# Optimization experiments

Measured on AMD Instinct MI355X. Metric: run time of the kernel, lower is better.

## Reference

```python
import jax, jax.numpy as jnp
import numpy as np
from functools import partial

B, INPUT_DIM, CHUNK, D, NLAYERS, FF, NCLS = 16, 20480, 10, 256, 4, 1024, 10
L = INPUT_DIM // CHUNK  # 2048
FILT_EMB, FILT_HID = 16, 64
EPS = 1e-5


def sinusoidal_pe(length, dim):
    pos = jnp.arange(length, dtype=jnp.float32)[:, None]
    div = jnp.exp(jnp.arange(0, dim, 2, dtype=jnp.float32) * (-np.log(10000.0) / dim))
    ang = pos * div  # (length, dim//2)
    pe = jnp.zeros((length, dim), dtype=jnp.float32)
    pe = pe.at[:, 0::2].set(jnp.sin(ang)).at[:, 1::2].set(jnp.cos(ang))
    return pe


def layernorm(x, g, b):
    mu = jnp.mean(x, axis=-1, keepdims=True)
    var = jnp.mean(jnp.square(x - mu), axis=-1, keepdims=True)
    return (x - mu) * jax.lax.rsqrt(var + EPS) * g + b


def setup_inputs() -> dict:
    key = jax.random.key(0)
    ks = iter(jax.random.split(key, 32))
    s = 0.02
    r = lambda shape: jax.random.normal(next(ks), shape, dtype=jnp.float32) * s
    inp = {
        'x': jax.random.normal(next(ks), (B, INPUT_DIM), dtype=jnp.float32),
        'inp_w': r((CHUNK, D)), 'inp_b': jnp.zeros((D,)),
        'in_proj_w': r((NLAYERS, D, 3 * D)), 'in_proj_b': jnp.zeros((NLAYERS, 3 * D)),
        'short_w': r((NLAYERS, D, 3)), 'short_b': jnp.zeros((NLAYERS, D)),
        'filt_w1': r((NLAYERS, FILT_EMB, FILT_HID)), 'filt_b1': jnp.zeros((NLAYERS, FILT_HID)),
        'filt_w2': r((NLAYERS, FILT_HID, D)), 'filt_b2': jnp.zeros((NLAYERS, D)),
        'out_w': r((NLAYERS, D, D)), 'out_b': jnp.zeros((NLAYERS, D)),
        'ln1_g': jnp.ones((NLAYERS, D)), 'ln1_b': jnp.zeros((NLAYERS, D)),
        'ln2_g': jnp.ones((NLAYERS, D)), 'ln2_b': jnp.zeros((NLAYERS, D)),
        'ffn_w1': r((NLAYERS, D, FF)), 'ffn_b1': jnp.zeros((NLAYERS, FF)),
        'ffn_w2': r((NLAYERS, FF, D)), 'ffn_b2': jnp.zeros((NLAYERS, D)),
        'norm_g': jnp.ones((D,)), 'norm_b': jnp.zeros((D,)),
        'cls_w': r((D, NCLS)), 'cls_b': jnp.zeros((NCLS,)),
    }
    return inp


def _hyena_op(u, in_w, in_b, sw, sb, fw1, fb1, fw2, fb2, ow, ob, pe16):
    # u: (B, L, D)
    proj = u @ in_w + in_b                       # (B, L, 3D)
    x0, x1, x2 = jnp.split(proj, 3, axis=-1)
    # depthwise short conv, kernel 3, same padding
    x0t = jnp.transpose(x0, (0, 2, 1))           # (B, D, L)
    x0c = jax.lax.conv_general_dilated(
        x0t, sw[:, None, :], window_strides=(1,), padding=[(1, 1)],
        feature_group_count=D, dimension_numbers=('NCH', 'OIH', 'NCH'))
    x0c = jnp.transpose(x0c + sb[None, :, None], (0, 2, 1))  # (B, L, D)
    # implicit long filter from positional MLP
    h = jax.nn.gelu(pe16 @ fw1 + fb1, approximate=False) @ fw2 + fb2  # (L, D)
    # FFT causal-style long conv (n = 2L)
    xf = jnp.fft.rfft(x0c, n=2 * L, axis=1)
    hf = jnp.fft.rfft(h, n=2 * L, axis=0)
    y = jnp.fft.irfft(xf * hf[None], n=2 * L, axis=1)[:, :L, :]
    y = y * x1 * x2                              # elementwise gating
    return y @ ow + ob


def reference(x, inp_w, inp_b, in_proj_w, in_proj_b, short_w, short_b,
              filt_w1, filt_b1, filt_w2, filt_b2, out_w, out_b,
              ln1_g, ln1_b, ln2_g, ln2_b, ffn_w1, ffn_b1, ffn_w2, ffn_b2,
              norm_g, norm_b, cls_w, cls_b):
    xs = x.reshape(B, L, CHUNK) @ inp_w + inp_b  # (B, L, D)
    xs = xs + sinusoidal_pe(L, D)[None]
    pe16 = sinusoidal_pe(L, FILT_EMB)
    for i in range(NLAYERS):
        h = _hyena_op(layernorm(xs, ln1_g[i], ln1_b[i]),
                      in_proj_w[i], in_proj_b[i], short_w[i], short_b[i],
                      filt_w1[i], filt_b1[i], filt_w2[i], filt_b2[i],
                      out_w[i], out_b[i], pe16)
        xs = xs + h
        z = layernorm(xs, ln2_g[i], ln2_b[i])
        z = jax.nn.gelu(z @ ffn_w1[i] + ffn_b1[i], approximate=False) @ ffn_w2[i] + ffn_b2[i]
        xs = xs + z
    pooled = layernorm(jnp.mean(xs, axis=1), norm_g, norm_b)
    return pooled @ cls_w + cls_b
```

## Files before the change

kernel.cpp:

```cpp
#include <hip/hip_runtime.h>
#include <math.h>

#define BB 16
#define LL 2048
#define CHUNK 10
#define DD 256
#define NLAYERS 4
#define FFD 1024
#define NCLS 10
#define HSTRC 2056

typedef short bf16x8 __attribute__((ext_vector_type(8)));
typedef short s16x4 __attribute__((ext_vector_type(4)));
typedef float f32x4 __attribute__((ext_vector_type(4)));

__device__ __forceinline__ unsigned short f2bf(float f) {
    unsigned int u = __builtin_bit_cast(unsigned int, f);
    u = (u + 0x7FFF + ((u >> 16) & 1)) >> 16;
    return (unsigned short)u;
}
__device__ __forceinline__ float bf2f(unsigned short s) {
    unsigned int u = ((unsigned int)s) << 16;
    return __builtin_bit_cast(float, u);
}
__device__ __forceinline__ float bfLO(unsigned v) { return __builtin_bit_cast(float, v << 16); }
__device__ __forceinline__ float bfHI(unsigned v) { return __builtin_bit_cast(float, v & 0xFFFF0000u); }

#define PADC(a) ((a) + ((a) >> 4))

__device__ __forceinline__ float2 cmulf(float2 a, float2 b) {
    return make_float2(fmaf(-a.y, b.y, a.x * b.x), fmaf(a.y, b.x, a.x * b.y));
}

#define GLL16(gsrc, ldst) \
    __builtin_amdgcn_global_load_lds((const __attribute__((address_space(1))) void*)(gsrc), \
                                     (__attribute__((address_space(3))) void*)(ldst), 16, 0, 0)

__global__ __launch_bounds__(256)
void embed_k(const float* __restrict__ x, const float* __restrict__ iw,
             const float* __restrict__ ib, float* __restrict__ xs)
{
    const int tid = threadIdx.x;
    const size_t row0 = (size_t)blockIdx.x * 8;
    const int i2 = (tid >> 1) * 2;
    const float div = expf(-0.03597789207803197f * (float)i2);
    float wcol[CHUNK];
#pragma unroll
    for (int c = 0; c < CHUNK; ++c) wcol[c] = iw[c * DD + tid];
    const float bv = ib[tid];
    for (int rr = 0; rr < 8; ++rr) {
        size_t row = row0 + rr;
        int l = (int)(row & (LL - 1));
        const float* xr = x + row * CHUNK;
        float acc = bv;
#pragma unroll
        for (int c = 0; c < CHUNK; ++c) acc += xr[c] * wcol[c];
        float sv, cv;
        sincosf((float)l * div, &sv, &cv);
        acc += (tid & 1) ? cv : sv;
        xs[row * DD + tid] = acc;
    }
}

__global__ __launch_bounds__(256)
void filt_k(const float* __restrict__ fw1, const float* __restrict__ fb1,
            const float* __restrict__ fw2, const float* __restrict__ fb2,
            float* __restrict__ hT)
{
    __shared__ float pe[16];
    __shared__ float hid[64];
    const int tid = threadIdx.x, l = blockIdx.x;
    if (tid < 16) {
        int i2 = (tid >> 1) * 2;
        float div = expf(-0.5756462732485114f * (float)i2);
        float sv, cv;
        sincosf((float)l * div, &sv, &cv);
        pe[tid] = (tid & 1) ? cv : sv;
    }
    __syncthreads();
    if (tid < 64) {
        float a = fb1[tid];
#pragma unroll
        for (int e = 0; e < 16; ++e) a += pe[e] * fw1[e * 64 + tid];
        hid[tid] = 0.5f * a * (1.0f + erff(a * 0.70710678118f));
    }
    __syncthreads();
    float a = fb2[tid];
#pragma unroll
    for (int h = 0; h < 64; ++h) a += hid[h] * fw2[h * DD + tid];
    hT[(size_t)tid * LL + l] = a;
}

__device__ __forceinline__ void dft4c(float2 a, float2 b, float2 c, float2 d,
                                      float2& F0, float2& F1, float2& F2, float2& F3)
{
    float t0r = a.x + c.x, t0i = a.y + c.y;
    float t1r = a.x - c.x, t1i = a.y - c.y;
    float t2r = b.x + d.x, t2i = b.y + d.y;
    float t3r = b.x - d.x, t3i = b.y - d.y;
    F0 = make_float2(t0r + t2r, t0i + t2i);
    F2 = make_float2(t0r - t2r, t0i - t2i);
    F1 = make_float2(t1r + t3i, t1i - t3r);
    F3 = make_float2(t1r - t3i, t1i + t3r);
}

template <int SH>
__device__ __forceinline__ void stage8ip(float2* __restrict__ A, int tid)
{
    constexpr int ST = 1 << SH;
    const int p = tid >> SH;
    const int q = tid & (ST - 1);
    float2 x0 = A[PADC(tid)];
    float2 x1 = A[PADC(tid + 256)];
    float2 x2 = A[PADC(tid + 512)];
    float2 x3 = A[PADC(tid + 768)];
    float2 x4 = A[PADC(tid + 1024)];
    float2 x5 = A[PADC(tid + 1280)];
    float2 x6 = A[PADC(tid + 1536)];
    float2 x7 = A[PADC(tid + 1792)];
    float2 E0, E1, E2, E3, O0, O1, O2, O3;
    dft4c(x0, x2, x4, x6, E0, E1, E2, E3);
    dft4c(x1, x3, x5, x7, O0, O1, O2, O3);
    const float C8 = 0.70710678118654752f;
    float2 y0 = make_float2(E0.x + O0.x, E0.y + O0.y);
    float2 y4 = make_float2(E0.x - O0.x, E0.y - O0.y);
    float a1 = C8 * (O1.x + O1.y), b1 = C8 * (O1.y - O1.x);
    float2 y1 = make_float2(E1.x + a1, E1.y + b1);
    float2 y5 = make_float2(E1.x - a1, E1.y - b1);
    float2 y2 = make_float2(E2.x + O2.y, E2.y - O2.x);
    float2 y6 = make_float2(E2.x - O2.y, E2.y + O2.x);
    float a3 = -C8 * (O3.x - O3.y), b3 = -C8 * (O3.x + O3.y);
    float2 y3 = make_float2(E3.x + a3, E3.y + b3);
    float2 y7 = make_float2(E3.x - a3, E3.y - b3);
    const int k0 = p << SH;
    float s1, c1;
    __sincosf(-3.0679615757712823e-3f * (float)k0, &s1, &c1);
    float2 w1 = make_float2(c1, s1);
    float2 w2 = cmulf(w1, w1);
    float2 w3 = cmulf(w2, w1);
    float2 w4 = cmulf(w2, w2);
    float2 w5 = cmulf(w3, w2);
    float2 w6 = cmulf(w3, w3);
    float2 w7 = cmulf(w4, w3);
    float2 o1 = cmulf(w1, y1);
    float2 o2 = cmulf(w2, y2);
    float2 o3 = cmulf(w3, y3);
    float2 o4 = cmulf(w4, y4);
    float2 o5 = cmulf(w5, y5);
    float2 o6 = cmulf(w6, y6);
    float2 o7 = cmulf(w7, y7);
    __syncthreads();
    const int ob = q + ((ST * p) << 3);
    A[PADC(ob)] = y0;
    A[PADC(ob + ST)] = o1;
    A[PADC(ob + 2 * ST)] = o2;
    A[PADC(ob + 3 * ST)] = o3;
    A[PADC(ob + 4 * ST)] = o4;
    A[PADC(ob + 5 * ST)] = o5;
    A[PADC(ob + 6 * ST)] = o6;
    A[PADC(ob + 7 * ST)] = o7;
    __syncthreads();
}

__device__ __forceinline__ void stage4fip(float2* __restrict__ A, int tid)
{
    float2 v[2][4];
#pragma unroll
    for (int jj = 0; jj < 2; ++jj) {
        int u = tid + (jj << 8);
        v[jj][0] = A[PADC(u)];
        v[jj][1] = A[PADC(u + 512)];
        v[jj][2] = A[PADC(u + 1024)];
        v[jj][3] = A[PADC(u + 1536)];
    }
    __syncthreads();
#pragma unroll
    for (int jj = 0; jj < 2; ++jj) {
        int u = tid + (jj << 8);
        float2 F0, F1, F2, F3;
        dft4c(v[jj][0], v[jj][1], v[jj][2], v[jj][3], F0, F1, F2, F3);
        A[PADC(u)] = F0;
        A[PADC(u + 512)] = F1;
        A[PADC(u + 1024)] = F2;
        A[PADC(u + 1536)] = F3;
    }
    __syncthreads();
}

__device__ __forceinline__ void fft2048ip(float2* __restrict__ A, int tid)
{
    stage8ip<0>(A, tid);
    stage8ip<3>(A, tid);
    stage8ip<6>(A, tid);
    stage4fip(A, tid);
}

__global__ __launch_bounds__(256)
void ffth_k(const float* __restrict__ hT, float2* __restrict__ Hf)
{
    __shared__ float2 A2[2176];
    const int tid = threadIdx.x, d = blockIdx.x;
    const float2* rowf = reinterpret_cast<const float2*>(hT + (size_t)d * LL);
#pragma unroll
    for (int j = 0; j < 4; ++j) {
        int u = tid + (j << 8);
        A2[PADC(u)] = rowf[u];
        A2[PADC(u + 1024)] = make_float2(0.0f, 0.0f);
    }
    __syncthreads();
    fft2048ip(A2, tid);
    float2* hf = Hf + (size_t)d * HSTRC;
#pragma unroll
    for (int j = 0; j < 4; ++j) {
        int k = 1 + tid + (j << 8);
        int m = 2048 - k;
        float2 zk = A2[PADC(k)], zm = A2[PADC(m)];
        float Er = 0.5f * (zk.x + zm.x), Ei = 0.5f * (zk.y - zm.y);
        float Or = 0.5f * (zk.y + zm.y), Oi = -0.5f * (zk.x - zm.x);
        float ts, tc;
        __sincosf(-1.5339807878856412e-3f * (float)k, &ts, &tc);
        float TOr = tc * Or - ts * Oi, TOi = tc * Oi + ts * Or;
        hf[k] = make_float2(Er + TOr, Ei + TOi);
        hf[m] = make_float2(Er - TOr, -(Ei - TOi));
    }
    if (tid == 0) {
        float2 z0 = A2[PADC(0)];
        hf[0] = make_float2(z0.x + z0.y, z0.x - z0.y);
    }
}

__global__ __launch_bounds__(256, 4)
void fftconv_k(const unsigned short* __restrict__ x0T, unsigned short* __restrict__ yT,
               const float2* __restrict__ Hf, const float* __restrict__ sw,
               const float* __restrict__ sb)
{
    __shared__ float2 A2[2176];
    const int tid = threadIdx.x;
    const int w = blockIdx.x;
    const int c = w & 7, s = w >> 3;
    const int d = c * 32 + (s & 31);
    const int b = s >> 5;
    const int blk = b * 256 + d;
    const float w0 = sw[d * 3], w1 = sw[d * 3 + 1], w2 = sw[d * 3 + 2];
    const float bv = sb[d];

    float* rawF = reinterpret_cast<float*>(A2);
    {
        const uint4* rowv = reinterpret_cast<const uint4*>(x0T + (size_t)blk * LL);
        uint4 ld = rowv[tid];
        int p = tid << 3;
        int lB = p & ~63;
        int p6 = p & 63;
        int fg = p6 >> 4;
        int m0 = (p6 >> 2) & 3;
        float4* d0 = reinterpret_cast<float4*>(rawF + lB + m0 * 16 + fg * 4);
        float4* d1 = reinterpret_cast<float4*>(rawF + lB + (m0 + 1) * 16 + fg * 4);
        *d0 = make_float4(bfLO(ld.x), bfHI(ld.x), bfLO(ld.y), bfHI(ld.y));
        *d1 = make_float4(bfLO(ld.z), bfHI(ld.z), bfLO(ld.w), bfHI(ld.w));
    }
    __syncthreads();
    float2 zv[4];
#pragma unroll
    for (int j = 0; j < 4; ++j) {
        int u = tid + (j << 8);
        float xm1 = (u == 0) ? 0.0f : rawF[2 * u - 1];
        float xc0 = rawF[2 * u];
        float xp1 = rawF[2 * u + 1];
        float xp2 = (u == 1023) ? 0.0f : rawF[2 * u + 2];
        zv[j].x = bv + w0 * xm1 + w1 * xc0 + w2 * xp1;
        zv[j].y = bv + w0 * xc0 + w1 * xp1 + w2 * xp2;
    }
    __syncthreads();
#pragma unroll
    for (int j = 0; j < 4; ++j) {
        int u = tid + (j << 8);
        A2[PADC(u)] = zv[j];
        A2[PADC(u + 1024)] = make_float2(0.0f, 0.0f);
    }
    __syncthreads();
    fft2048ip(A2, tid);
    const float2* hf = Hf + (size_t)d * HSTRC;
#pragma unroll
    for (int j = 0; j < 4; ++j) {
        int k = 1 + tid + (j << 8);
        int m = 2048 - k;
        float2 zk = A2[PADC(k)], zm = A2[PADC(m)];
        float Er = 0.5f * (zk.x + zm.x), Ei = 0.5f * (zk.y - zm.y);
        float Or = 0.5f * (zk.y + zm.y), Oi = -0.5f * (zk.x - zm.x);
        float ts, tc;
        __sincosf(-1.5339807878856412e-3f * (float)k, &ts, &tc);
        float TOr = tc * Or - ts * Oi, TOi = tc * Oi + ts * Or;
        float Xpr = Er + TOr, Xpi = Ei + TOi;
        float Xmr = Er - TOr, Xmi = Ei - TOi;
        float2 hk = hf[k], hm = hf[m];
        float Ykr = Xpr * hk.x - Xpi * hk.y, Yki = Xpr * hk.y + Xpi * hk.x;
        float Cr = Xmr * hm.x + Xmi * hm.y, Ci = Xmi * hm.x - Xmr * hm.y;
        float Pr = 0.5f * (Ykr + Cr), Pi = 0.5f * (Yki + Ci);
        float Gr = 0.5f * (Ykr - Cr), Gi = 0.5f * (Yki - Ci);
        float Qr = tc * Gr + ts * Gi, Qi = tc * Gi - ts * Gr;
        A2[PADC(k)] = make_float2(Pr - Qi, -(Pi + Qr));
        A2[PADC(m)] = make_float2(Pr + Qi, Pi - Qr);
    }
    if (tid == 0) {
        float2 z0 = A2[PADC(0)];
        float2 h0 = hf[0];
        float X0 = z0.x + z0.y, X2 = z0.x - z0.y;
        float Y0 = X0 * h0.x, Y2 = X2 * h0.y;
        float P = 0.5f * (Y0 + Y2), Q = 0.5f * (Y0 - Y2);
        A2[PADC(0)] = make_float2(P, -Q);
    }
    __syncthreads();
    fft2048ip(A2, tid);
    const float sc = 1.0f / 2048.0f;
    unsigned* yrow = reinterpret_cast<unsigned*>(yT + (size_t)blk * LL);
#pragma unroll
    for (int j = 0; j < 4; ++j) {
        int u = tid + (j << 8);
        float2 v = A2[PADC(u)];
        float e = v.x * sc, o = -v.y * sc;
        yrow[u] = (unsigned)f2bf(e) | ((unsigned)f2bf(o) << 16);
    }
}

__global__ __launch_bounds__(256)
void gate_k(const unsigned short* __restrict__ yTb, const unsigned short* __restrict__ px,
            unsigned short* __restrict__ yg)
{
    __shared__ float t[64][65];
    const int tid = threadIdx.x;
    const int blk = blockIdx.x;
    const int b = blk >> 7;
    const int dt = (blk >> 5) & 3;
    const int lt = blk & 31;
    const int d0 = dt << 6, l0 = lt << 6;
    const int r0 = tid >> 6, c = tid & 63;
    for (int rr = 0; rr < 16; ++rr) {
        int dl = rr * 4 + r0;
        t[dl][c] = bf2f(yTb[(((size_t)(b << 8) + d0 + dl) << 11) + l0 + c]);
    }
    __syncthreads();
    const int lid = tid & 63, lr = tid >> 6;
    for (int k = 0; k < 16; ++k) {
        int ll = k * 4 + lr;
        int l = l0 + ll;
        size_t pb = ((size_t)(b * LL + l)) * 512;
        float v = t[lid][ll];
        float x1 = bf2f(px[pb + d0 + lid]);
        float x2 = bf2f(px[pb + 256 + d0 + lid]);
        yg[((size_t)(b * LL + l)) * DD + d0 + lid] = f2bf(v * x1 * x2);
    }
}

__global__ __launch_bounds__(256)
void lncast_k(const float* __restrict__ xs, const float* __restrict__ g,
              const float* __restrict__ b, unsigned short* __restrict__ o)
{
    const int tid = threadIdx.x, lane = tid & 63, wave = tid >> 6;
    const size_t row = (size_t)blockIdx.x * 4 + wave;
    float4 v = reinterpret_cast<const float4*>(xs + row * DD)[lane];
    float s = v.x + v.y + v.z + v.w;
#pragma unroll
    for (int off = 32; off > 0; off >>= 1) s += __shfl_xor(s, off, 64);
    float mean = s * (1.0f / 256.0f);
    float e0 = v.x - mean, e1 = v.y - mean, e2 = v.z - mean, e3 = v.w - mean;
    float q = e0 * e0 + e1 * e1 + e2 * e2 + e3 * e3;
#pragma unroll
    for (int off = 32; off > 0; off >>= 1) q += __shfl_xor(q, off, 64);
    float rstd = rsqrtf(q * (1.0f / 256.0f) + 1e-5f);
    float4 gg = reinterpret_cast<const float4*>(g)[lane];
    float4 bb = reinterpret_cast<const float4*>(b)[lane];
    s16x4 r;
    r[0] = (short)f2bf(e0 * rstd * gg.x + bb.x);
    r[1] = (short)f2bf(e1 * rstd * gg.y + bb.y);
    r[2] = (short)f2bf(e2 * rstd * gg.z + bb.z);
    r[3] = (short)f2bf(e3 * rstd * gg.w + bb.w);
    *reinterpret_cast<s16x4*>(o + row * DD + lane * 4) = r;
}

__global__ __launch_bounds__(256)
void wcastT_k(const float* __restrict__ W, unsigned short* __restrict__ WT, int K, int N)
{
    __shared__ float t[32][33];
    const int tx = threadIdx.x & 31, ty = threadIdx.x >> 5;
    const int n0 = blockIdx.x * 32, k0 = blockIdx.y * 32;
#pragma unroll
    for (int j = 0; j < 4; ++j)
        t[ty + 8 * j][tx] = W[(size_t)(k0 + ty + 8 * j) * N + n0 + tx];
    __syncthreads();
#pragma unroll
    for (int j = 0; j < 4; ++j)
        WT[(size_t)(n0 + ty + 8 * j) * K + k0 + tx] = f2bf(t[tx][ty + 8 * j]);
}

template <int K, int N, int MODE>
__global__ __launch_bounds__(256)
void gemm_k(const unsigned short* __restrict__ A, const unsigned short* __restrict__ WT,
            const float* __restrict__ bias, void* __restrict__ outp, void* __restrict__ outp2)
{
    constexpr int C = N / 128;
    __shared__ unsigned short ldsA[8192];
    __shared__ unsigned short ldsB[8192];
    const int tid = threadIdx.x;
    const int lane = tid & 63, wid = tid >> 6;
    const int nwg = gridDim.x;
    const int w = blockIdx.x;
    const int logical = (w & 7) * (nwg >> 3) + (w >> 3);
    const int row0 = (logical / C) * 128;
    const int col0 = (logical % C) * 128;
    const int wm = (wid >> 1) * 64, wn = (wid & 1) * 64;
    const int fr = lane & 15, fg = lane >> 4;

    f32x4 acc[4][4];
#pragma unroll
    for (int n = 0; n < 4; ++n) {
        float bv = bias[col0 + wn + n * 16 + fr];
#pragma unroll
        for (int m = 0; m < 4; ++m) {
            acc[m][n][0] = bv; acc[m][n][1] = bv; acc[m][n][2] = bv; acc[m][n][3] = bv;
        }
    }

    const int srow = wid * 8 + (lane >> 3);
    const int sc = lane & 7;

    for (int kt = 0; kt < K / 64; ++kt) {
        const int k0 = kt * 64;
#pragma unroll
        for (int it = 0; it < 4; ++it) {
            int row = it * 32 + srow;
            int cs = sc ^ (row & 7);
            const char* ga = (const char*)(A + (size_t)(row0 + row) * K + k0) + cs * 16;
            const char* gb = (const char*)(WT + (size_t)(col0 + row) * K + k0) + cs * 16;
            GLL16(ga, (char*)ldsA + it * 4096 + wid * 1024);
            GLL16(gb, (char*)ldsB + it * 4096 + wid * 1024);
        }
        __syncthreads();
#pragma unroll
        for (int ks = 0; ks < 2; ++ks) {
            bf16x8 af[4], bf[4];
#pragma unroll
            for (int m = 0; m < 4; ++m) {
                int ar = wm + m * 16 + fr;
                int slot = (ks * 4 + fg) ^ (ar & 7);
                af[m] = *reinterpret_cast<const bf16x8*>(ldsA + ar * 64 + slot * 8);
            }
#pragma unroll
            for (int n = 0; n < 4; ++n) {
                int br = wn + n * 16 + fr;
                int slot = (ks * 4 + fg) ^ (br & 7);
                bf[n] = *reinterpret_cast<const bf16x8*>(ldsB + br * 64 + slot * 8);
            }
#pragma unroll
            for (int m = 0; m < 4; ++m)
#pragma unroll
                for (int n = 0; n < 4; ++n)
                    acc[m][n] = __builtin_amdgcn_mfma_f32_16x16x32_bf16(af[m], bf[n], acc[m][n], 0, 0, 0);
        }
        __syncthreads();
    }

    if constexpr (MODE == 3) {
        if (col0 < 256) {
            const int b = row0 >> 11;
            const int lb0 = (row0 & (LL - 1)) + wm;
#pragma unroll
            for (int n = 0; n < 4; ++n) {
                int dcol = col0 + wn + n * 16 + fr;
                unsigned short* dst = (unsigned short*)outp +
                    (((size_t)(b << 8) + dcol) << 11) + lb0 + fg * 16;
                unsigned pk[8];
#pragma unroll
                for (int q = 0; q < 8; ++q) {
                    int m = q >> 1, r0 = (q & 1) * 2;
                    pk[q] = (unsigned)f2bf(acc[m][n][r0]) | ((unsigned)f2bf(acc[m][n][r0 + 1]) << 16);
                }
                *reinterpret_cast<uint4*>(dst)     = make_uint4(pk[0], pk[1], pk[2], pk[3]);
                *reinterpret_cast<uint4*>(dst + 8) = make_uint4(pk[4], pk[5], pk[6], pk[7]);
            }
        } else {
            unsigned short* px = (unsigned short*)outp2;
#pragma unroll
            for (int m = 0; m < 4; ++m) {
                int gr = row0 + wm + m * 16 + fg * 4;
#pragma unroll
                for (int n = 0; n < 4; ++n) {
                    int gc = col0 - 256 + wn + n * 16 + fr;
#pragma unroll
                    for (int r = 0; r < 4; ++r)
                        px[(size_t)(gr + r) * 512 + gc] = f2bf(acc[m][n][r]);
                }
            }
        }
        return;
    }

#pragma unroll
    for (int m = 0; m < 4; ++m) {
        int gr = row0 + wm + m * 16 + fg * 4;
#pragma unroll
        for (int n = 0; n < 4; ++n) {
            int gc = col0 + wn + n * 16 + fr;
#pragma unroll
            for (int r = 0; r < 4; ++r) {
                float v = acc[m][n][r];
                if constexpr (MODE == 1) v = 0.5f * v * (1.0f + erff(v * 0.70710678118f));
                if constexpr (MODE <= 1) {
                    ((unsigned short*)outp)[(size_t)(gr + r) * N + gc] = f2bf(v);
                } else {
                    float* o = (float*)outp + (size_t)(gr + r) * N + gc;
                    *o += v;
                }
            }
        }
    }
}

template <int K>
__global__ __launch_bounds__(256)
void gemm_ln_k(const unsigned short* __restrict__ A, const unsigned short* __restrict__ WT,
               const float* __restrict__ bias, const float* __restrict__ lng,
               const float* __restrict__ lnb, float* __restrict__ xs,
               unsigned short* __restrict__ xln)
{
    __shared__ unsigned short ldsA[64 * 64];
    __shared__ unsigned short ldsB[256 * 64];
    const int tid = threadIdx.x;
    const int lane = tid & 63, wid = tid >> 6;
    const int nwg = gridDim.x;
    const int w = blockIdx.x;
    const int logical = (w & 7) * (nwg >> 3) + (w >> 3);
    const size_t row0 = (size_t)logical * 64;
    const int fr = lane & 15, fg = lane >> 4;

    f32x4 acc[16];
#pragma unroll
    for (int n = 0; n < 16; ++n) {
        float bv = bias[n * 16 + fr];
        acc[n][0] = bv; acc[n][1] = bv; acc[n][2] = bv; acc[n][3] = bv;
    }

    for (int kt = 0; kt < K / 64; ++kt) {
        const int k0 = kt * 64;
#pragma unroll
        for (int p = 0; p < 2; ++p) {
            int cch = p * 256 + tid;
            int row = cch >> 3;
            int cs = (cch & 7) ^ (row & 7);
            const char* ga = (const char*)(A + (row0 + row) * K + k0) + cs * 16;
            GLL16(ga, (char*)ldsA + p * 4096 + wid * 1024);
        }
#pragma unroll
        for (int p = 0; p < 8; ++p) {
            int cch = p * 256 + tid;
            int row = cch >> 3;
            int cs = (cch & 7) ^ (row & 7);
            const char* gb = (const char*)(WT + (size_t)row * K + k0) + cs * 16;
            GLL16(gb, (char*)ldsB + p * 4096 + wid * 1024);
        }
        __syncthreads();
#pragma unroll
        for (int ks = 0; ks < 2; ++ks) {
            int ar = wid * 16 + fr;
            int slotA = (ks * 4 + fg) ^ (ar & 7);
            bf16x8 af = *reinterpret_cast<const bf16x8*>(ldsA + ar * 64 + slotA * 8);
#pragma unroll
            for (int n = 0; n < 16; ++n) {
                int br = n * 16 + fr;
                int slotB = (ks * 4 + fg) ^ (br & 7);
                bf16x8 bf = *reinterpret_cast<const bf16x8*>(ldsB + br * 64 + slotB * 8);
                acc[n] = __builtin_amdgcn_mfma_f32_16x16x32_bf16(af, bf, acc[n], 0, 0, 0);
            }
        }
        __syncthreads();
    }

    const size_t rbase = row0 + wid * 16 + fg * 4;
#pragma unroll
    for (int r = 0; r < 4; ++r) {
        const float* xr = xs + (rbase + r) * DD;
#pragma unroll
        for (int n = 0; n < 16; ++n)
            acc[n][r] += xr[fr + 16 * n];
    }
    float sm[4], sq[4];
#pragma unroll
    for (int r = 0; r < 4; ++r) {
        float s = 0.0f, q = 0.0f;
#pragma unroll
        for (int n = 0; n < 16; ++n) {
            float v = acc[n][r];
            s += v; q += v * v;
        }
#pragma unroll
        for (int off = 1; off < 16; off <<= 1) {
            s += __shfl_xor(s, off, 64);
            q += __shfl_xor(q, off, 64);
        }
        sm[r] = s * (1.0f / 256.0f);
        float var = q * (1.0f / 256.0f) - sm[r] * sm[r];
        sq[r] = rsqrtf(var + 1e-5f);
    }
    float gv[16], bvv[16];
#pragma unroll
    for (int n = 0; n < 16; ++n) {
        gv[n] = lng[fr + 16 * n];
        bvv[n] = lnb[fr + 16 * n];
    }
#pragma unroll
    for (int r = 0; r < 4; ++r) {
        float* xw = xs + (rbase + r) * DD;
        unsigned short* lw = xln + (rbase + r) * DD;
#pragma unroll
        for (int n = 0; n < 16; ++n) {
            int gc = fr + 16 * n;
            float v = acc[n][r];
            xw[gc] = v;
            lw[gc] = f2bf((v - sm[r]) * sq[r] * gv[n] + bvv[n]);
        }
    }
}

__global__ __launch_bounds__(256)
void pool_k(const float* __restrict__ xs, float* __restrict__ part)
{
    const int tid = threadIdx.x;
    const int b = blockIdx.x >> 4, g = blockIdx.x & 15;
    size_t base = ((size_t)b * LL + g * 128) * DD + tid;
    float s = 0.0f;
    for (int l = 0; l < 128; ++l) s += xs[base + (size_t)l * DD];
    part[(size_t)blockIdx.x * DD + tid] = s;
}

__global__ __launch_bounds__(256)
void final_k(const float* __restrict__ part, const float* __restrict__ ng,
             const float* __restrict__ nb, const float* __restrict__ cw,
             const float* __restrict__ cb, float* __restrict__ out)
{
    __shared__ float pl[256];
    __shared__ float red[4], red2[4];
    const int tid = threadIdx.x, b = blockIdx.x;
    float m = 0.0f;
    for (int g = 0; g < 16; ++g) m += part[((size_t)b * 16 + g) * DD + tid];
    m *= (1.0f / (float)LL);
    const int lane = tid & 63, wave = tid >> 6;
    float s = m;
#pragma unroll
    for (int off = 32; off > 0; off >>= 1) s += __shfl_xor(s, off, 64);
    if (lane == 0) red[wave] = s;
    __syncthreads();
    float mean = (red[0] + red[1] + red[2] + red[3]) * (1.0f / 256.0f);
    float dm = m - mean;
    float qv = dm * dm;
#pragma unroll
    for (int off = 32; off > 0; off >>= 1) qv += __shfl_xor(qv, off, 64);
    if (lane == 0) red2[wave] = qv;
    __syncthreads();
    float var = (red2[0] + red2[1] + red2[2] + red2[3]) * (1.0f / 256.0f);
    pl[tid] = dm * rsqrtf(var + 1e-5f) * ng[tid] + nb[tid];
    __syncthreads();
    if (tid < NCLS) {
        float a = cb[tid];
        for (int dd = 0; dd < 256; ++dd) a += pl[dd] * cw[dd * NCLS + tid];
        out[b * NCLS + tid] = a;
    }
}

extern "C" void kernel_launch(void* const* d_in, const int* in_sizes, int n_in,
                              void* d_out, int out_size, void* d_ws, size_t ws_size,
                              hipStream_t stream)
{
    (void)in_sizes; (void)n_in; (void)out_size; (void)ws_size;
    const float* x        = (const float*)d_in[0];
    const float* inp_w    = (const float*)d_in[1];
    const float* inp_b    = (const float*)d_in[2];
    const float* in_proj_w= (const float*)d_in[3];
    const float* in_proj_b= (const float*)d_in[4];
    const float* short_w  = (const float*)d_in[5];
    const float* short_b  = (const float*)d_in[6];
    const float* filt_w1  = (const float*)d_in[7];
    const float* filt_b1  = (const float*)d_in[8];
    const float* filt_w2  = (const float*)d_in[9];
    const float* filt_b2  = (const float*)d_in[10];
    const float* out_w    = (const float*)d_in[11];
    const float* out_b    = (const float*)d_in[12];
    const float* ln1_g    = (const float*)d_in[13];
    const float* ln1_b    = (const float*)d_in[14];
    const float* ln2_g    = (const float*)d_in[15];
    const float* ln2_b    = (const float*)d_in[16];
    const float* ffn_w1   = (const float*)d_in[17];
    const float* ffn_b1   = (const float*)d_in[18];
    const float* ffn_w2   = (const float*)d_in[19];
    const float* ffn_b2   = (const float*)d_in[20];
    const float* norm_g   = (const float*)d_in[21];
    const float* norm_b   = (const float*)d_in[22];
    const float* cls_w    = (const float*)d_in[23];
    const float* cls_b    = (const float*)d_in[24];

    float* ws = (float*)d_ws;
    float* xs            = ws;
    unsigned short* xln  = (unsigned short*)(ws + 8388608);
    unsigned short* x0T  = (unsigned short*)(ws + 12582912);
    unsigned short* yT   = (unsigned short*)(ws + 16777216);
    unsigned short* projx= (unsigned short*)(ws + 20971520);
    unsigned short* ygp  = x0T;
    unsigned short* hid  = x0T;
    float* hT            = ws + 29360128;
    float2* Hf           = (float2*)(ws + 29884416);
    float* part          = ws + 30937088;
    unsigned short* WTb  = (unsigned short*)(ws + 31002624);

    for (int i = 0; i < NLAYERS; ++i) {
        unsigned short* wt = WTb + (size_t)i * 786432;
        wcastT_k<<<dim3(24, 8), 256, 0, stream>>>(in_proj_w + (size_t)i * 196608, wt, 256, 768);
        wcastT_k<<<dim3(8, 8), 256, 0, stream>>>(out_w + (size_t)i * 65536, wt + 196608, 256, 256);
        wcastT_k<<<dim3(32, 8), 256, 0, stream>>>(ffn_w1 + (size_t)i * 262144, wt + 262144, 256, 1024);
        wcastT_k<<<dim3(8, 32), 256, 0, stream>>>(ffn_w2 + (size_t)i * 262144, wt + 524288, 1024, 256);
    }

    embed_k<<<4096, 256, 0, stream>>>(x, inp_w, inp_b, xs);
    lncast_k<<<8192, 256, 0, stream>>>(xs, ln1_g, ln1_b, xln);

    for (int i = 0; i < NLAYERS; ++i) {
        unsigned short* wt = WTb + (size_t)i * 786432;
        filt_k<<<LL, 256, 0, stream>>>(filt_w1 + i * 1024, filt_b1 + i * 64,
                                       filt_w2 + i * 16384, filt_b2 + i * 256, hT);
        ffth_k<<<DD, 256, 0, stream>>>(hT, Hf);
        gemm_k<256, 768, 3><<<1536, 256, 0, stream>>>(
            xln, wt, in_proj_b + i * 768, x0T, projx);
        fftconv_k<<<4096, 256, 0, stream>>>(x0T, yT, Hf, short_w + i * 768, short_b + i * 256);
        gate_k<<<2048, 256, 0, stream>>>(yT, projx, ygp);
        gemm_ln_k<256><<<512, 256, 0, stream>>>(
            ygp, wt + 196608, out_b + i * 256, ln2_g + i * 256, ln2_b + i * 256, xs, xln);
        gemm_k<256, 1024, 1><<<2048, 256, 0, stream>>>(
            xln, wt + 262144, ffn_b1 + i * 1024, hid, nullptr);
        if (i < NLAYERS - 1) {
            gemm_ln_k<1024><<<512, 256, 0, stream>>>(
                hid, wt + 524288, ffn_b2 + i * 256,
                ln1_g + (i + 1) * 256, ln1_b + (i + 1) * 256, xs, xln);
        } else {
            gemm_k<1024, 256, 2><<<512, 256, 0, stream>>>(
                hid, wt + 524288, ffn_b2 + i * 256, xs, nullptr);
        }
    }

    pool_k<<<BB * 16, 256, 0, stream>>>(xs, part);
    final_k<<<BB, 256, 0, stream>>>(part, norm_g, norm_b, cls_w, cls_b, (float*)d_out);
}
```

Measured before the change: 788.1 us.

## Fuse FFN up-projection, GELU and down-projection into one kernel

Replaces the two FFN GEMM launches with a single kernel. Each 64-row block computes 128-column chunks of the hidden activation in registers, applies GELU, stages the result as bf16 in shared memory and accumulates straight into the down-projection. This removes the global write and re-read of the 32768x1024 hidden tensor and one launch per layer. In exchange each block streams both weight matrices itself, occupancy drops because of the larger shared-memory footprint, and there are many syncthreads with no double buffering of the weight tiles.

```diff
diff --git a/kernel.cpp b/kernel.cpp
--- a/kernel.cpp
+++ b/kernel.cpp
@@ -620,6 +620,168 @@
     }
 }
 
+template <bool DO_LN>
+__global__ __launch_bounds__(256)
+void ffn_fused_k(const unsigned short* __restrict__ xin, const unsigned short* __restrict__ WT1,
+                 const unsigned short* __restrict__ WT2, const float* __restrict__ b1,
+                 const float* __restrict__ b2, const float* __restrict__ lng,
+                 const float* __restrict__ lnb, float* __restrict__ xs,
+                 unsigned short* __restrict__ xln)
+{
+    __shared__ unsigned short wtile[16384];
+    __shared__ unsigned short hidl[8192];
+    const int tid = threadIdx.x;
+    const int lane = tid & 63, wv = tid >> 6;
+    const int nwg = gridDim.x;
+    const int w = blockIdx.x;
+    const int logical = (w & 7) * (nwg >> 3) + (w >> 3);
+    const size_t row0 = (size_t)logical * 64;
+    const int fr = lane & 15, fg = lane >> 4;
+
+    bf16x8 areg[8];
+    {
+        const unsigned short* arow = xin + (row0 + wv * 16 + fr) * DD;
+#pragma unroll
+        for (int t = 0; t < 8; ++t)
+            areg[t] = *reinterpret_cast<const bf16x8*>(arow + t * 32 + fg * 8);
+    }
+
+    f32x4 acc2[16];
+#pragma unroll
+    for (int n = 0; n < 16; ++n) {
+        float bv = b2[n * 16 + fr];
+        acc2[n][0] = bv; acc2[n][1] = bv; acc2[n][2] = bv; acc2[n][3] = bv;
+    }
+
+    for (int c = 0; c < 8; ++c) {
+        f32x4 acc1[8];
+#pragma unroll
+        for (int hm = 0; hm < 8; ++hm) {
+            float4 bq = *reinterpret_cast<const float4*>(b1 + c * 128 + hm * 16 + fg * 4);
+            acc1[hm][0] = bq.x; acc1[hm][1] = bq.y; acc1[hm][2] = bq.z; acc1[hm][3] = bq.w;
+        }
+#pragma unroll
+        for (int kt = 0; kt < 4; ++kt) {
+#pragma unroll
+            for (int it = 0; it < 4; ++it) {
+                int row = it * 32 + wv * 8 + (lane >> 3);
+                int cs = (lane & 7) ^ (row & 7);
+                const char* g1 = (const char*)(WT1 + (size_t)(c * 128 + row) * 256 + kt * 64) + cs * 16;
+                GLL16(g1, (char*)wtile + it * 4096 + wv * 1024);
+            }
+            __syncthreads();
+#pragma unroll
+            for (int ks = 0; ks < 2; ++ks) {
+#pragma unroll
+                for (int hm = 0; hm < 8; ++hm) {
+                    int br = hm * 16 + fr;
+                    int slot = (ks * 4 + fg) ^ (br & 7);
+                    bf16x8 w1f = *reinterpret_cast<const bf16x8*>(wtile + br * 64 + slot * 8);
+                    acc1[hm] = __builtin_amdgcn_mfma_f32_16x16x32_bf16(w1f, areg[kt * 2 + ks], acc1[hm], 0, 0, 0);
+                }
+            }
+            __syncthreads();
+        }
+        {
+            const int hrow = wv * 16 + fr;
+#pragma unroll
+            for (int hm = 0; hm < 8; ++hm) {
+                float g0 = acc1[hm][0], g1v = acc1[hm][1], g2 = acc1[hm][2], g3 = acc1[hm][3];
+                g0 = 0.5f * g0 * (1.0f + erff(g0 * 0.70710678118f));
+                g1v = 0.5f * g1v * (1.0f + erff(g1v * 0.70710678118f));
+                g2 = 0.5f * g2 * (1.0f + erff(g2 * 0.70710678118f));
+                g3 = 0.5f * g3 * (1.0f + erff(g3 * 0.70710678118f));
+                uint2 pk;
+                pk.x = (unsigned)f2bf(g0) | ((unsigned)f2bf(g1v) << 16);
+                pk.y = (unsigned)f2bf(g2) | ((unsigned)f2bf(g3) << 16);
+                int byteoff = hrow * 256 + ((hm * 32 + fg * 8) ^ ((fr & 7) << 4));
+                *reinterpret_cast<uint2*>((char*)hidl + byteoff) = pk;
+            }
+        }
+        __syncthreads();
+#pragma unroll
+        for (int kt2 = 0; kt2 < 2; ++kt2) {
+#pragma unroll
+            for (int p = 0; p < 8; ++p) {
+                int cch = p * 256 + tid;
+                int row = cch >> 3;
+                int cs = (cch & 7) ^ (row & 7);
+                const char* g2p = (const char*)(WT2 + (size_t)row * 1024 + c * 128 + kt2 * 64) + cs * 16;
+                GLL16(g2p, (char*)wtile + p * 4096 + wv * 1024);
+            }
+            __syncthreads();
+#pragma unroll
+            for (int ks = 0; ks < 2; ++ks) {
+                int kbyte = (wv * 16 + fr) * 256 + ((kt2 * 128 + ks * 64 + fg * 16) ^ ((fr & 7) << 4));
+                bf16x8 af = *reinterpret_cast<const bf16x8*>((const char*)hidl + kbyte);
+#pragma unroll
+                for (int n = 0; n < 16; ++n) {
+                    int br = n * 16 + fr;
+                    int slot = (ks * 4 + fg) ^ (br & 7);
+                    bf16x8 bfv = *reinterpret_cast<const bf16x8*>(wtile + br * 64 + slot * 8);
+                    acc2[n] = __builtin_amdgcn_mfma_f32_16x16x32_bf16(af, bfv, acc2[n], 0, 0, 0);
+                }
+            }
+            __syncthreads();
+        }
+    }
+
+    const size_t rbase = row0 + wv * 16 + fg * 4;
+#pragma unroll
+    for (int r = 0; r < 4; ++r) {
+        const float* xr = xs + (rbase + r) * DD;
+#pragma unroll
+        for (int n = 0; n < 16; ++n)
+            acc2[n][r] += xr[fr + 16 * n];
+    }
+    if constexpr (DO_LN) {
+        float sm[4], sq[4];
+#pragma unroll
+        for (int r = 0; r < 4; ++r) {
+            float s = 0.0f, q = 0.0f;
+#pragma unroll
+            for (int n = 0; n < 16; ++n) {
+                float v = acc2[n][r];
+                s += v; q += v * v;
+            }
+#pragma unroll
+            for (int off = 1; off < 16; off <<= 1) {
+                s += __shfl_xor(s, off, 64);
+                q += __shfl_xor(q, off, 64);
+            }
+            sm[r] = s * (1.0f / 256.0f);
+            float var = q * (1.0f / 256.0f) - sm[r] * sm[r];
+            sq[r] = rsqrtf(var + 1e-5f);
+        }
+        float gv[16], bvv[16];
+#pragma unroll
+        for (int n = 0; n < 16; ++n) {
+            gv[n] = lng[fr + 16 * n];
+            bvv[n] = lnb[fr + 16 * n];
+        }
+#pragma unroll
+        for (int r = 0; r < 4; ++r) {
+            float* xw = xs + (rbase + r) * DD;
+            unsigned short* lw = xln + (rbase + r) * DD;
+#pragma unroll
+            for (int n = 0; n < 16; ++n) {
+                int gc = fr + 16 * n;
+                float v = acc2[n][r];
+                xw[gc] = v;
+                lw[gc] = f2bf((v - sm[r]) * sq[r] * gv[n] + bvv[n]);
+            }
+        }
+    } else {
+#pragma unroll
+        for (int r = 0; r < 4; ++r) {
+            float* xw = xs + (rbase + r) * DD;
+#pragma unroll
+            for (int n = 0; n < 16; ++n)
+                xw[fr + 16 * n] = acc2[n][r];
+        }
+    }
+}
+
 __global__ __launch_bounds__(256)
 void pool_k(const float* __restrict__ xs, float* __restrict__ part)
 {
@@ -703,7 +865,6 @@
     unsigned short* yT   = (unsigned short*)(ws + 16777216);
     unsigned short* projx= (unsigned short*)(ws + 20971520);
     unsigned short* ygp  = x0T;
-    unsigned short* hid  = x0T;
     float* hT            = ws + 29360128;
     float2* Hf           = (float2*)(ws + 29884416);
     float* part          = ws + 30937088;
@@ -731,15 +892,14 @@
         gate_k<<<2048, 256, 0, stream>>>(yT, projx, ygp);
         gemm_ln_k<256><<<512, 256, 0, stream>>>(
             ygp, wt + 196608, out_b + i * 256, ln2_g + i * 256, ln2_b + i * 256, xs, xln);
-        gemm_k<256, 1024, 1><<<2048, 256, 0, stream>>>(
-            xln, wt + 262144, ffn_b1 + i * 1024, hid, nullptr);
         if (i < NLAYERS - 1) {
-            gemm_ln_k<1024><<<512, 256, 0, stream>>>(
-                hid, wt + 524288, ffn_b2 + i * 256,
+            ffn_fused_k<true><<<512, 256, 0, stream>>>(
+                xln, wt + 262144, wt + 524288, ffn_b1 + i * 1024, ffn_b2 + i * 256,
                 ln1_g + (i + 1) * 256, ln1_b + (i + 1) * 256, xs, xln);
         } else {
-            gemm_k<1024, 256, 2><<<512, 256, 0, stream>>>(
-                hid, wt + 524288, ffn_b2 + i * 256, xs, nullptr);
+            ffn_fused_k<false><<<512, 256, 0, stream>>>(
+                xln, wt + 262144, wt + 524288, ffn_b1 + i * 1024, ffn_b2 + i * 256,
+                nullptr, nullptr, xs, nullptr);
         }
     }
 
```

New measurement: 828.4 us. 1.05x slower.

## Batch weight casts and filter FFTs across layers; pack two signals per fftconv block

Applied to the files above, without the earlier changes.

Merges the 16 per-layer weight-transpose launches into one kernel, and computes the implicit filters and their FFTs for all four layers up front in single launches instead of once per layer. This removes launch overhead and small, underfilled grids. The fftconv kernel now runs 512 threads per block, each half handling one channel with its own LDS buffer, which halves the block count. The trade-off is more workspace memory and a different occupancy profile for fftconv, since the launch_bounds min-blocks hint was dropped.

```diff
diff --git a/kernel.cpp b/kernel.cpp
--- a/kernel.cpp
+++ b/kernel.cpp
@@ -63,13 +63,19 @@
 }
 
 __global__ __launch_bounds__(256)
-void filt_k(const float* __restrict__ fw1, const float* __restrict__ fb1,
-            const float* __restrict__ fw2, const float* __restrict__ fb2,
-            float* __restrict__ hT)
+void filt_all_k(const float* __restrict__ fw1, const float* __restrict__ fb1,
+                const float* __restrict__ fw2, const float* __restrict__ fb2,
+                float* __restrict__ hTall)
 {
     __shared__ float pe[16];
     __shared__ float hid[64];
-    const int tid = threadIdx.x, l = blockIdx.x;
+    const int tid = threadIdx.x;
+    const int layer = blockIdx.x >> 11;
+    const int l = blockIdx.x & 2047;
+    const float* w1 = fw1 + layer * 1024;
+    const float* b1 = fb1 + layer * 64;
+    const float* w2 = fw2 + layer * 16384;
+    const float* b2 = fb2 + layer * 256;
     if (tid < 16) {
         int i2 = (tid >> 1) * 2;
         float div = expf(-0.5756462732485114f * (float)i2);
@@ -79,16 +85,16 @@
     }
     __syncthreads();
     if (tid < 64) {
-        float a = fb1[tid];
-#pragma unroll
-        for (int e = 0; e < 16; ++e) a += pe[e] * fw1[e * 64 + tid];
+        float a = b1[tid];
+#pragma unroll
+        for (int e = 0; e < 16; ++e) a += pe[e] * w1[e * 64 + tid];
         hid[tid] = 0.5f * a * (1.0f + erff(a * 0.70710678118f));
     }
     __syncthreads();
-    float a = fb2[tid];
-#pragma unroll
-    for (int h = 0; h < 64; ++h) a += hid[h] * fw2[h * DD + tid];
-    hT[(size_t)tid * LL + l] = a;
+    float a = b2[tid];
+#pragma unroll
+    for (int h = 0; h < 64; ++h) a += hid[h] * w2[h * DD + tid];
+    hTall[(size_t)layer * 524288 + (size_t)tid * LL + l] = a;
 }
 
 __device__ __forceinline__ void dft4c(float2 a, float2 b, float2 c, float2 d,
@@ -196,11 +202,13 @@
 }
 
 __global__ __launch_bounds__(256)
-void ffth_k(const float* __restrict__ hT, float2* __restrict__ Hf)
+void ffth_all_k(const float* __restrict__ hTall, float2* __restrict__ Hfall)
 {
     __shared__ float2 A2[2176];
-    const int tid = threadIdx.x, d = blockIdx.x;
-    const float2* rowf = reinterpret_cast<const float2*>(hT + (size_t)d * LL);
+    const int tid = threadIdx.x;
+    const int layer = blockIdx.x >> 8;
+    const int d = blockIdx.x & 255;
+    const float2* rowf = reinterpret_cast<const float2*>(hTall + (size_t)layer * 524288 + (size_t)d * LL);
 #pragma unroll
     for (int j = 0; j < 4; ++j) {
         int u = tid + (j << 8);
@@ -209,7 +217,7 @@
     }
     __syncthreads();
     fft2048ip(A2, tid);
-    float2* hf = Hf + (size_t)d * HSTRC;
+    float2* hf = Hfall + ((size_t)layer * 256 + d) * HSTRC;
 #pragma unroll
     for (int j = 0; j < 4; ++j) {
         int k = 1 + tid + (j << 8);
@@ -229,17 +237,19 @@
     }
 }
 
-__global__ __launch_bounds__(256, 4)
+__global__ __launch_bounds__(512)
 void fftconv_k(const unsigned short* __restrict__ x0T, unsigned short* __restrict__ yT,
                const float2* __restrict__ Hf, const float* __restrict__ sw,
                const float* __restrict__ sb)
 {
-    __shared__ float2 A2[2176];
-    const int tid = threadIdx.x;
+    __shared__ float2 A2d[2][2176];
+    const int sig = threadIdx.x >> 8;
+    const int tid = threadIdx.x & 255;
+    float2* A2 = A2d[sig];
     const int w = blockIdx.x;
     const int c = w & 7, s = w >> 3;
-    const int d = c * 32 + (s & 31);
-    const int b = s >> 5;
+    const int d = c * 32 + (s & 15) * 2 + sig;
+    const int b = s >> 4;
     const int blk = b * 256 + d;
     const float w0 = sw[d * 3], w1 = sw[d * 3 + 1], w2 = sw[d * 3 + 2];
     const float bv = sb[d];
@@ -378,11 +388,26 @@
 }
 
 __global__ __launch_bounds__(256)
-void wcastT_k(const float* __restrict__ W, unsigned short* __restrict__ WT, int K, int N)
-{
+void wcast_all_k(const float* __restrict__ in_proj_w, const float* __restrict__ out_w,
+                 const float* __restrict__ ffn_w1, const float* __restrict__ ffn_w2,
+                 unsigned short* __restrict__ WTb)
+{
+    const int bid = blockIdx.x;
+    const int layer = bid / 768;
+    const int r = bid % 768;
+    const float* W; unsigned short* WT; int K, N, nt, kt;
+    unsigned short* wt = WTb + (size_t)layer * 786432;
+    if (r < 192)      { int i = r;       nt = i % 24; kt = i / 24; K = 256;  N = 768;
+                        W = in_proj_w + (size_t)layer * 196608; WT = wt; }
+    else if (r < 256) { int i = r - 192; nt = i % 8;  kt = i / 8;  K = 256;  N = 256;
+                        W = out_w + (size_t)layer * 65536;      WT = wt + 196608; }
+    else if (r < 512) { int i = r - 256; nt = i % 32; kt = i / 32; K = 256;  N = 1024;
+                        W = ffn_w1 + (size_t)layer * 262144;    WT = wt + 262144; }
+    else              { int i = r - 512; nt = i % 8;  kt = i / 8;  K = 1024; N = 256;
+                        W = ffn_w2 + (size_t)layer * 262144;    WT = wt + 524288; }
     __shared__ float t[32][33];
     const int tx = threadIdx.x & 31, ty = threadIdx.x >> 5;
-    const int n0 = blockIdx.x * 32, k0 = blockIdx.y * 32;
+    const int n0 = nt * 32, k0 = kt * 32;
 #pragma unroll
     for (int j = 0; j < 4; ++j)
         t[ty + 8 * j][tx] = W[(size_t)(k0 + ty + 8 * j) * N + n0 + tx];
@@ -704,30 +729,23 @@
     unsigned short* projx= (unsigned short*)(ws + 20971520);
     unsigned short* ygp  = x0T;
     unsigned short* hid  = x0T;
-    float* hT            = ws + 29360128;
-    float2* Hf           = (float2*)(ws + 29884416);
-    float* part          = ws + 30937088;
-    unsigned short* WTb  = (unsigned short*)(ws + 31002624);
+    float* hTall         = ws + 29360128;
+    float2* Hfall        = (float2*)(ws + 31457280);
+    float* part          = ws + 35667968;
+    unsigned short* WTb  = (unsigned short*)(ws + 35733504);
+
+    wcast_all_k<<<3072, 256, 0, stream>>>(in_proj_w, out_w, ffn_w1, ffn_w2, WTb);
+    embed_k<<<4096, 256, 0, stream>>>(x, inp_w, inp_b, xs);
+    lncast_k<<<8192, 256, 0, stream>>>(xs, ln1_g, ln1_b, xln);
+    filt_all_k<<<NLAYERS * 2048, 256, 0, stream>>>(filt_w1, filt_b1, filt_w2, filt_b2, hTall);
+    ffth_all_k<<<NLAYERS * 256, 256, 0, stream>>>(hTall, Hfall);
 
     for (int i = 0; i < NLAYERS; ++i) {
         unsigned short* wt = WTb + (size_t)i * 786432;
-        wcastT_k<<<dim3(24, 8), 256, 0, stream>>>(in_proj_w + (size_t)i * 196608, wt, 256, 768);
-        wcastT_k<<<dim3(8, 8), 256, 0, stream>>>(out_w + (size_t)i * 65536, wt + 196608, 256, 256);
-        wcastT_k<<<dim3(32, 8), 256, 0, stream>>>(ffn_w1 + (size_t)i * 262144, wt + 262144, 256, 1024);
-        wcastT_k<<<dim3(8, 32), 256, 0, stream>>>(ffn_w2 + (size_t)i * 262144, wt + 524288, 1024, 256);
-    }
-
-    embed_k<<<4096, 256, 0, stream>>>(x, inp_w, inp_b, xs);
-    lncast_k<<<8192, 256, 0, stream>>>(xs, ln1_g, ln1_b, xln);
-
-    for (int i = 0; i < NLAYERS; ++i) {
-        unsigned short* wt = WTb + (size_t)i * 786432;
-        filt_k<<<LL, 256, 0, stream>>>(filt_w1 + i * 1024, filt_b1 + i * 64,
-                                       filt_w2 + i * 16384, filt_b2 + i * 256, hT);
-        ffth_k<<<DD, 256, 0, stream>>>(hT, Hf);
+        float2* Hf = Hfall + (size_t)i * 256 * HSTRC;
         gemm_k<256, 768, 3><<<1536, 256, 0, stream>>>(
             xln, wt, in_proj_b + i * 768, x0T, projx);
-        fftconv_k<<<4096, 256, 0, stream>>>(x0T, yT, Hf, short_w + i * 768, short_b + i * 256);
+        fftconv_k<<<2048, 512, 0, stream>>>(x0T, yT, Hf, short_w + i * 768, short_b + i * 256);
         gate_k<<<2048, 256, 0, stream>>>(yT, projx, ygp);
         gemm_ln_k<256><<<512, 256, 0, stream>>>(
             ygp, wt + 196608, out_b + i * 256, ln2_g + i * 256, ln2_b + i * 256, xs, xln);
```

Result: slower. 806.8 us (+2.4%).
